# Performance work log

Hardware: AMD Instinct MI355X
Metric: run time of the kernel (lower is better)

## Reference

```python
import jax, jax.numpy as jnp
import numpy as np

N = 10000      # num nodes
E = 320000     # num edges
IN = 256       # in_dim
MP = 256       # mp_width
FL = 512       # fl_width
OUT = 64       # out_dim


def setup_inputs() -> dict:
    key = jax.random.key(0)
    ks = jax.random.split(key, 20)
    inp = {}
    inp["x"] = jax.random.normal(ks[0], (N, IN), dtype=jnp.float32)
    inp["edge_index"] = jax.random.randint(ks[1], (2, E), 0, N, dtype=jnp.int64)
    # iMP (frozen) linear layers: weight ~ N(0, 1) per nn.init.normal_(std=1.0)
    inp["mp_w0"] = jax.random.normal(ks[2], (IN, MP), dtype=jnp.float32)
    inp["mp_b0"] = jax.random.uniform(ks[3], (MP,), minval=-1.0, maxval=1.0) / np.sqrt(IN)
    inp["mp_w1"] = jax.random.normal(ks[4], (MP, MP), dtype=jnp.float32)
    inp["mp_b1"] = jax.random.uniform(ks[5], (MP,), minval=-1.0, maxval=1.0) / np.sqrt(MP)
    inp["mp_w2"] = jax.random.normal(ks[6], (MP, MP), dtype=jnp.float32)
    inp["mp_b2"] = jax.random.uniform(ks[7], (MP,), minval=-1.0, maxval=1.0) / np.sqrt(MP)
    # FC layers (torch default Linear init scale ~ 1/sqrt(fan_in))
    inp["fc_w0"] = jax.random.normal(ks[8], (MP, FL), dtype=jnp.float32) / np.sqrt(MP)
    inp["fc_b0"] = jnp.zeros((FL,), dtype=jnp.float32)
    inp["fc_w1"] = jax.random.normal(ks[9], (FL, FL), dtype=jnp.float32) / np.sqrt(FL)
    inp["fc_b1"] = jnp.zeros((FL,), dtype=jnp.float32)
    # injection projections
    inp["inj_w0"] = jax.random.normal(ks[10], (MP, FL), dtype=jnp.float32) / np.sqrt(MP)
    inp["inj_b0"] = jnp.zeros((FL,), dtype=jnp.float32)
    inp["inj_w1"] = jax.random.normal(ks[11], (MP, FL), dtype=jnp.float32) / np.sqrt(MP)
    inp["inj_b1"] = jnp.zeros((FL,), dtype=jnp.float32)
    inp["alpha"] = jnp.array(1.0, dtype=jnp.float32)
    inp["out_w"] = jax.random.normal(ks[12], (FL, OUT), dtype=jnp.float32) / np.sqrt(FL)
    inp["out_b"] = jnp.zeros((OUT,), dtype=jnp.float32)
    return inp


def _imp(x, w, b, row, col, deg_inv):
    # h = relu(W x); h /= deg; Ah = scatter_add over row of h[col]
    h = jax.nn.relu(x @ w + b) * deg_inv[:, None]      # [N, out]
    return jnp.zeros_like(h).at[row].add(h[col])       # gather + scatter-add


def reference(x, edge_index, mp_w0, mp_b0, mp_w1, mp_b1, mp_w2, mp_b2,
              fc_w0, fc_b0, fc_w1, fc_b1, inj_w0, inj_b0, inj_w1, inj_b1,
              alpha, out_w, out_b):
    row, col = edge_index[0], edge_index[1]
    deg = jax.ops.segment_sum(jnp.ones((E,), x.dtype), col, num_segments=N)
    # nodes with deg==0 never appear in col so clamping does not change output
    deg_inv = 1.0 / jnp.maximum(deg, 1.0)

    h = _imp(x, mp_w0, mp_b0, row, col, deg_inv)
    h = _imp(h, mp_w1, mp_b1, row, col, deg_inv)
    h = _imp(h, mp_w2, mp_b2, row, col, deg_inv)

    x_inject = h
    h = alpha * (jax.nn.relu(h) @ fc_w0 + fc_b0) + (x_inject @ inj_w0 + inj_b0)
    h = alpha * (jax.nn.relu(h) @ fc_w1 + fc_b1) + (x_inject @ inj_w1 + inj_b1)
    return h @ out_w + out_b
```

## Files before the change

kernel.cpp:

```cpp
#include <hip/hip_runtime.h>

#define N_NODES 10000
#define N_EDGES 320000
#define MPAD 10112
#define NBIN 10048
#define CAP 128
#define EBLKS 157
#define PREP_BLOCKS 512
#define PREP_TOT 1148480L

typedef unsigned short u16;
typedef short bf16x8 __attribute__((ext_vector_type(8)));
typedef float f32x4 __attribute__((ext_vector_type(4)));

__device__ __forceinline__ u16 f2b(float f) {
  unsigned u = __builtin_bit_cast(unsigned, f);
  unsigned r = u + 0x7fffu + ((u >> 16) & 1u);
  return (u16)(r >> 16);
}
__device__ __forceinline__ unsigned pack2(float a, float b) {
  return (unsigned)f2b(a) | ((unsigned)f2b(b) << 16);
}
__device__ __forceinline__ float blo(unsigned u) { return __builtin_bit_cast(float, u << 16); }
__device__ __forceinline__ float bhi(unsigned u) { return __builtin_bit_cast(float, u & 0xffff0000u); }

struct PP {
  const float *x; const int *ei;
  const float *w0, *w1, *w2, *fcw0, *injw0, *fcw1, *injw1, *outw;
  const float *fcb0, *injb0, *fcb1, *injb1, *alpha, *outb;
  u16 *xb, *w0t, *w1t, *w2t, *wc1t, *wft;
  float *bias1, *bf;
  int *cursor, *deg, *csr;
};

__global__ __launch_bounds__(256) void prep_place(PP P) {
  const int tid = threadIdx.x, bid = blockIdx.x;

  if (bid < EBLKS) {
    const int e0 = bid * 2048;
#pragma unroll
    for (int j = 0; j < 2048; j += 256) {
      int e = e0 + j + tid;
      if (e < N_EDGES) {
        int r = P.ei[e];
        int c = P.ei[N_EDGES + e];
        int pos = atomicAdd(&P.cursor[r], 1);
        if (pos < CAP) P.csr[r * CAP + pos] = c;
        atomicAdd(&P.deg[c], 1);
      }
    }
    return;
  }

  const float alpha = P.alpha[0];
  const long stride = (long)PREP_BLOCKS * 256;
  for (long ii = (long)(bid - EBLKS) * 256 + tid; ii < PREP_TOT; ii += stride) {
    long i = ii;
    if (i < 640000L) {
      float4 v = ((const float4*)P.x)[i];
      uint2 o;
      o.x = pack2(v.x, v.y);
      o.y = pack2(v.z, v.w);
      *(uint2*)(P.xb + 4 * i) = o;
      continue;
    }
    i -= 640000L;
    if (i < 65536) { P.w0t[i] = f2b(P.w0[(i & 255) * 256 + (i >> 8)]); continue; }
    i -= 65536;
    if (i < 65536) { P.w1t[i] = f2b(P.w1[(i & 255) * 256 + (i >> 8)]); continue; }
    i -= 65536;
    if (i < 65536) { P.w2t[i] = f2b(P.w2[(i & 255) * 256 + (i >> 8)]); continue; }
    i -= 65536;
    if (i < 262144) {
      int n = (int)(i >> 9), k = (int)(i & 511);
      float v = (k < 256) ? alpha * P.fcw0[k * 512 + n] : P.injw0[(k - 256) * 512 + n];
      P.wc1t[i] = f2b(v); continue;
    }
    i -= 262144;
    if (i < 49152) {
      int n = (int)(i & 63), k = (int)(i >> 6);
      const float* fr = (k < 512) ? P.fcw1 + (size_t)k * 512
                                  : P.injw1 + (size_t)(k - 512) * 512;
      float a0 = 0.f, a1 = 0.f, a2 = 0.f, a3 = 0.f;
#pragma unroll 4
      for (int j = 0; j < 512; j += 4) {
        float4 f = *(const float4*)(fr + j);
        a0 += f.x * P.outw[(j + 0) * 64 + n];
        a1 += f.y * P.outw[(j + 1) * 64 + n];
        a2 += f.z * P.outw[(j + 2) * 64 + n];
        a3 += f.w * P.outw[(j + 3) * 64 + n];
      }
      float acc = (a0 + a1) + (a2 + a3);
      if (k < 512) acc *= alpha;
      P.wft[n * 768 + k] = f2b(acc);
      continue;
    }
    i -= 49152;
    if (i < 64) {
      float acc = P.outb[i];
#pragma unroll 8
      for (int j = 0; j < 512; ++j)
        acc += (alpha * P.fcb1[j] + P.injb1[j]) * P.outw[j * 64 + i];
      P.bf[i] = acc;
      continue;
    }
    i -= 64;
    if (i < 512) { P.bias1[i] = alpha * P.fcb0[i] + P.injb0[i]; continue; }
  }
}

template<int K, bool RELU, bool SCALE, bool F32OUT>
__global__ __launch_bounds__(128) void gemm64(
    const u16* __restrict__ A, int lda,
    const u16* __restrict__ Bt,
    const float* __restrict__ bias,
    const int* __restrict__ deg,
    u16* __restrict__ Cb, float* __restrict__ Cf, int ldc)
{
  __shared__ u16 As[64 * 72];
  __shared__ u16 Bs[64 * 72];
  const int tid = threadIdx.x;
  const int m0 = blockIdx.x * 64;
  const int n0 = blockIdx.y * 64;
  const int wave = tid >> 6;
  const int lane = tid & 63;
  const int wr = wave * 32;
  const int lm = lane & 15;
  const int koff = (lane >> 4) * 8;

  const int srow = tid >> 2;
  const int scol = (tid & 3) * 16;
  const u16* Ag0 = A + (size_t)(m0 + srow) * lda + scol;
  const u16* Ag1 = A + (size_t)(m0 + srow + 32) * lda + scol;
  const u16* Bg0 = Bt + (size_t)(n0 + srow) * K + scol;
  const u16* Bg1 = Bt + (size_t)(n0 + srow + 32) * K + scol;
  u16* Asw0 = &As[srow * 72 + scol];
  u16* Asw1 = &As[(srow + 32) * 72 + scol];
  u16* Bsw0 = &Bs[srow * 72 + scol];
  u16* Bsw1 = &Bs[(srow + 32) * 72 + scol];

  f32x4 acc[2][4] = {};

  int4 pa0 = *(const int4*)(Ag0),     pa1 = *(const int4*)(Ag0 + 8);
  int4 pa2 = *(const int4*)(Ag1),     pa3 = *(const int4*)(Ag1 + 8);
  int4 pb0 = *(const int4*)(Bg0),     pb1 = *(const int4*)(Bg0 + 8);
  int4 pb2 = *(const int4*)(Bg1),     pb3 = *(const int4*)(Bg1 + 8);

#pragma unroll
  for (int kb = 0; kb < K; kb += 64) {
    __syncthreads();
    *(int4*)Asw0 = pa0; *(int4*)(Asw0 + 8) = pa1;
    *(int4*)Asw1 = pa2; *(int4*)(Asw1 + 8) = pa3;
    *(int4*)Bsw0 = pb0; *(int4*)(Bsw0 + 8) = pb1;
    *(int4*)Bsw1 = pb2; *(int4*)(Bsw1 + 8) = pb3;
    __syncthreads();
    if (kb + 64 < K) {
      pa0 = *(const int4*)(Ag0 + kb + 64); pa1 = *(const int4*)(Ag0 + kb + 72);
      pa2 = *(const int4*)(Ag1 + kb + 64); pa3 = *(const int4*)(Ag1 + kb + 72);
      pb0 = *(const int4*)(Bg0 + kb + 64); pb1 = *(const int4*)(Bg0 + kb + 72);
      pb2 = *(const int4*)(Bg1 + kb + 64); pb3 = *(const int4*)(Bg1 + kb + 72);
    }
#pragma unroll
    for (int ks = 0; ks < 2; ++ks) {
      bf16x8 af[2], bf[4];
#pragma unroll
      for (int mi = 0; mi < 2; ++mi)
        af[mi] = *(const bf16x8*)&As[(wr + mi * 16 + lm) * 72 + ks * 32 + koff];
#pragma unroll
      for (int ni = 0; ni < 4; ++ni)
        bf[ni] = *(const bf16x8*)&Bs[(ni * 16 + lm) * 72 + ks * 32 + koff];
#pragma unroll
      for (int mi = 0; mi < 2; ++mi)
#pragma unroll
        for (int ni = 0; ni < 4; ++ni)
          acc[mi][ni] = __builtin_amdgcn_mfma_f32_16x16x32_bf16(af[mi], bf[ni], acc[mi][ni], 0, 0, 0);
    }
  }

  const int q4 = (lane >> 4) * 4;
#pragma unroll
  for (int mi = 0; mi < 2; ++mi) {
#pragma unroll
    for (int ni = 0; ni < 4; ++ni) {
      const int gc = n0 + ni * 16 + lm;
      const float bv = bias[gc];
#pragma unroll
      for (int r = 0; r < 4; ++r) {
        const int gr = m0 + wr + mi * 16 + q4 + r;
        float v = acc[mi][ni][r] + bv;
        if (RELU) v = fmaxf(v, 0.f);
        if (SCALE) v *= 1.0f / fmaxf((float)deg[gr], 1.0f);
        if (F32OUT) {
          if (gr < N_NODES) Cf[(size_t)gr * ldc + gc] = v;
        } else {
          Cb[(size_t)gr * ldc + gc] = f2b(v);
        }
      }
    }
  }
}

__global__ __launch_bounds__(128) void gemm_fold(
    const u16* __restrict__ Ar,
    const u16* __restrict__ Ah,
    const u16* __restrict__ Bt,
    const float* __restrict__ bias,
    float* __restrict__ Cf)
{
  const int K = 768;
  __shared__ u16 As[64 * 72];
  __shared__ u16 Bs[64 * 72];
  const int tid = threadIdx.x;
  const int m0 = blockIdx.x * 64;
  const int n0 = 0;
  const int wave = tid >> 6;
  const int lane = tid & 63;
  const int wr = wave * 32;
  const int lm = lane & 15;
  const int koff = (lane >> 4) * 8;

  const int srow = tid >> 2;
  const int scol = (tid & 3) * 16;
  const int ar0 = m0 + srow, ar1 = m0 + srow + 32;
  auto aptr = [&](int row, int col) -> const u16* {
    return (col < 512) ? Ar + (size_t)row * 512 + col
                       : Ah + (size_t)row * 512 + (col - 512);
  };
  const u16* Bg0 = Bt + (size_t)(n0 + srow) * K + scol;
  const u16* Bg1 = Bt + (size_t)(n0 + srow + 32) * K + scol;
  u16* Asw0 = &As[srow * 72 + scol];
  u16* Asw1 = &As[(srow + 32) * 72 + scol];
  u16* Bsw0 = &Bs[srow * 72 + scol];
  u16* Bsw1 = &Bs[(srow + 32) * 72 + scol];

  f32x4 acc[2][4] = {};

  int4 pa0 = *(const int4*)aptr(ar0, scol);
  int4 pa1 = *(const int4*)aptr(ar0, scol + 8);
  int4 pa2 = *(const int4*)aptr(ar1, scol);
  int4 pa3 = *(const int4*)aptr(ar1, scol + 8);
  int4 pb0 = *(const int4*)(Bg0), pb1 = *(const int4*)(Bg0 + 8);
  int4 pb2 = *(const int4*)(Bg1), pb3 = *(const int4*)(Bg1 + 8);

#pragma unroll
  for (int kb = 0; kb < K; kb += 64) {
    __syncthreads();
    *(int4*)Asw0 = pa0; *(int4*)(Asw0 + 8) = pa1;
    *(int4*)Asw1 = pa2; *(int4*)(Asw1 + 8) = pa3;
    *(int4*)Bsw0 = pb0; *(int4*)(Bsw0 + 8) = pb1;
    *(int4*)Bsw1 = pb2; *(int4*)(Bsw1 + 8) = pb3;
    __syncthreads();
    if (kb + 64 < K) {
      int c = kb + 64 + scol;
      pa0 = *(const int4*)aptr(ar0, c);
      pa1 = *(const int4*)aptr(ar0, c + 8);
      pa2 = *(const int4*)aptr(ar1, c);
      pa3 = *(const int4*)aptr(ar1, c + 8);
      pb0 = *(const int4*)(Bg0 + kb + 64); pb1 = *(const int4*)(Bg0 + kb + 72);
      pb2 = *(const int4*)(Bg1 + kb + 64); pb3 = *(const int4*)(Bg1 + kb + 72);
    }
#pragma unroll
    for (int ks = 0; ks < 2; ++ks) {
      bf16x8 af[2], bf[4];
#pragma unroll
      for (int mi = 0; mi < 2; ++mi)
        af[mi] = *(const bf16x8*)&As[(wr + mi * 16 + lm) * 72 + ks * 32 + koff];
#pragma unroll
      for (int ni = 0; ni < 4; ++ni)
        bf[ni] = *(const bf16x8*)&Bs[(ni * 16 + lm) * 72 + ks * 32 + koff];
#pragma unroll
      for (int mi = 0; mi < 2; ++mi)
#pragma unroll
        for (int ni = 0; ni < 4; ++ni)
          acc[mi][ni] = __builtin_amdgcn_mfma_f32_16x16x32_bf16(af[mi], bf[ni], acc[mi][ni], 0, 0, 0);
    }
  }

  const int q4 = (lane >> 4) * 4;
#pragma unroll
  for (int mi = 0; mi < 2; ++mi) {
#pragma unroll
    for (int ni = 0; ni < 4; ++ni) {
      const int gc = ni * 16 + lm;
      const float bv = bias[gc];
#pragma unroll
      for (int r = 0; r < 4; ++r) {
        const int gr = m0 + wr + mi * 16 + q4 + r;
        if (gr < N_NODES) Cf[(size_t)gr * 64 + gc] = acc[mi][ni][r] + bv;
      }
    }
  }
}

__global__ __launch_bounds__(256) void aggregate(
    const u16* __restrict__ tmp, const int* __restrict__ cnt,
    const int* __restrict__ csr, u16* __restrict__ out0,
    u16* __restrict__ A1, int mode)
{
  const int wv = threadIdx.x >> 6;
  const int lane = threadIdx.x & 63;
  const int r = blockIdx.x * 4 + wv;
  const int half = lane >> 5;
  const int q = lane & 31;
  int n = cnt[r]; if (n > CAP) n = CAP;
  const int beg = r * CAP, end = beg + n;
  const size_t feat = (size_t)q * 16;
  const char* tb = (const char*)tmp;

  float s0 = 0.f, s1 = 0.f, s2 = 0.f, s3 = 0.f, s4 = 0.f, s5 = 0.f, s6 = 0.f, s7 = 0.f;
  int i = beg;
  for (; i + 8 <= end; i += 8) {
    uint4 v[4];
#pragma unroll
    for (int j = 0; j < 4; ++j)
      v[j] = *(const uint4*)(tb + (size_t)csr[i + 2 * j + half] * 512 + feat);
#pragma unroll
    for (int j = 0; j < 4; ++j) {
      s0 += blo(v[j].x); s1 += bhi(v[j].x); s2 += blo(v[j].y); s3 += bhi(v[j].y);
      s4 += blo(v[j].z); s5 += bhi(v[j].z); s6 += blo(v[j].w); s7 += bhi(v[j].w);
    }
  }
  for (; i < end; i += 2) {
    int id = i + half;
    if (id < end) {
      uint4 v = *(const uint4*)(tb + (size_t)csr[id] * 512 + feat);
      s0 += blo(v.x); s1 += bhi(v.x); s2 += blo(v.y); s3 += bhi(v.y);
      s4 += blo(v.z); s5 += bhi(v.z); s6 += blo(v.w); s7 += bhi(v.w);
    }
  }
  const int src = lane ^ 32;
  s0 += __shfl(s0, src, 64); s1 += __shfl(s1, src, 64);
  s2 += __shfl(s2, src, 64); s3 += __shfl(s3, src, 64);
  s4 += __shfl(s4, src, 64); s5 += __shfl(s5, src, 64);
  s6 += __shfl(s6, src, 64); s7 += __shfl(s7, src, 64);

  if (half == 0) {
    uint4 pv;
    pv.x = pack2(s0, s1); pv.y = pack2(s2, s3);
    pv.z = pack2(s4, s5); pv.w = pack2(s6, s7);
    if (mode == 0) {
      *(uint4*)((char*)out0 + (size_t)r * 512 + feat) = pv;
    } else {
      uint4 pr;
      pr.x = pack2(fmaxf(s0, 0.f), fmaxf(s1, 0.f));
      pr.y = pack2(fmaxf(s2, 0.f), fmaxf(s3, 0.f));
      pr.z = pack2(fmaxf(s4, 0.f), fmaxf(s5, 0.f));
      pr.w = pack2(fmaxf(s6, 0.f), fmaxf(s7, 0.f));
      *(uint4*)((char*)A1 + (size_t)r * 1024 + feat) = pr;
      *(uint4*)((char*)A1 + (size_t)r * 1024 + 512 + feat) = pv;
    }
  }
}

extern "C" void kernel_launch(void* const* d_in, const int* in_sizes, int n_in,
                              void* d_out, int out_size, void* d_ws, size_t ws_size,
                              hipStream_t stream) {
  const int* ei = (const int*)d_in[1];

  char* p = (char*)d_ws;
  auto carve = [&](size_t bytes) -> void* {
    void* r = (void*)p;
    p += (bytes + 255) & ~(size_t)255;
    return r;
  };
  int*   deg     = (int*)carve(MPAD * 4);
  int*   cursor  = (int*)carve(NBIN * 4);
  int*   csr     = (int*)carve((size_t)NBIN * CAP * 4);
  float* bias1   = (float*)carve(512 * 4);
  float* bf      = (float*)carve(64 * 4);
  u16* xb    = (u16*)carve((size_t)MPAD * 256 * 2);
  u16* w0t   = (u16*)carve(65536 * 2);
  u16* w1t   = (u16*)carve(65536 * 2);
  u16* w2t   = (u16*)carve(65536 * 2);
  u16* wc1t  = (u16*)carve(262144 * 2);
  u16* wft   = (u16*)carve(49152 * 2);
  u16* tmp   = (u16*)carve((size_t)MPAD * 256 * 2);
  u16* h     = (u16*)carve((size_t)MPAD * 256 * 2);
  u16* cat1  = (u16*)carve((size_t)MPAD * 512 * 2);
  u16* relu1 = (u16*)carve((size_t)MPAD * 512 * 2);

  PP pp;
  pp.x = (const float*)d_in[0];
  pp.ei = ei;
  pp.w0 = (const float*)d_in[2];
  pp.w1 = (const float*)d_in[4];
  pp.w2 = (const float*)d_in[6];
  pp.fcw0 = (const float*)d_in[8];
  pp.fcw1 = (const float*)d_in[10];
  pp.injw0 = (const float*)d_in[12];
  pp.injw1 = (const float*)d_in[14];
  pp.outw = (const float*)d_in[17];
  pp.fcb0 = (const float*)d_in[9];
  pp.injb0 = (const float*)d_in[13];
  pp.fcb1 = (const float*)d_in[11];
  pp.injb1 = (const float*)d_in[15];
  pp.alpha = (const float*)d_in[16];
  pp.outb = (const float*)d_in[18];
  pp.xb = xb; pp.w0t = w0t; pp.w1t = w1t; pp.w2t = w2t;
  pp.wc1t = wc1t; pp.wft = wft;
  pp.bias1 = bias1; pp.bf = bf;
  pp.cursor = cursor; pp.deg = deg; pp.csr = csr;

  const float* mp_b0 = (const float*)d_in[3];
  const float* mp_b1 = (const float*)d_in[5];
  const float* mp_b2 = (const float*)d_in[7];
  float* out = (float*)d_out;

  hipMemsetAsync(deg, 0, (size_t)(MPAD + NBIN) * 4, stream);
  prep_place<<<EBLKS + PREP_BLOCKS, 256, 0, stream>>>(pp);

  dim3 gmp(MPAD / 64, 4), gfc(MPAD / 64, 8), go(MPAD / 64, 1);
  gemm64<256, true, true, false><<<gmp, 128, 0, stream>>>(xb, 256, w0t, mp_b0, deg, tmp, nullptr, 256);
  aggregate<<<2500, 256, 0, stream>>>(tmp, cursor, csr, h, nullptr, 0);
  gemm64<256, true, true, false><<<gmp, 128, 0, stream>>>(h, 256, w1t, mp_b1, deg, tmp, nullptr, 256);
  aggregate<<<2500, 256, 0, stream>>>(tmp, cursor, csr, h, nullptr, 0);
  gemm64<256, true, true, false><<<gmp, 128, 0, stream>>>(h, 256, w2t, mp_b2, deg, tmp, nullptr, 256);
  aggregate<<<2500, 256, 0, stream>>>(tmp, cursor, csr, nullptr, cat1, 1);
  gemm64<512, true, false, false><<<gfc, 128, 0, stream>>>(cat1, 512, wc1t, bias1, nullptr, relu1, nullptr, 512);
  gemm_fold<<<go, 128, 0, stream>>>(relu1, cat1 + 256, wft, bf, out);
}
```

Before: 236.0 us.

## Fuse fp32-to-bf16 input conversion into first GEMM and shrink CSR to u16

```diff
diff --git a/kernel.cpp b/kernel.cpp
--- a/kernel.cpp
+++ b/kernel.cpp
@@ -7,7 +7,7 @@
 #define CAP 128
 #define EBLKS 157
 #define PREP_BLOCKS 512
-#define PREP_TOT 1148480L
+#define PREP_TOT 508480L
 
 typedef unsigned short u16;
 typedef short bf16x8 __attribute__((ext_vector_type(8)));
@@ -23,14 +23,20 @@
 }
 __device__ __forceinline__ float blo(unsigned u) { return __builtin_bit_cast(float, u << 16); }
 __device__ __forceinline__ float bhi(unsigned u) { return __builtin_bit_cast(float, u & 0xffff0000u); }
+__device__ __forceinline__ int4 cvt16(float4 a, float4 b) {
+  int4 r;
+  r.x = (int)pack2(a.x, a.y); r.y = (int)pack2(a.z, a.w);
+  r.z = (int)pack2(b.x, b.y); r.w = (int)pack2(b.z, b.w);
+  return r;
+}
 
 struct PP {
   const float *x; const int *ei;
   const float *w0, *w1, *w2, *fcw0, *injw0, *fcw1, *injw1, *outw;
   const float *fcb0, *injb0, *fcb1, *injb1, *alpha, *outb;
-  u16 *xb, *w0t, *w1t, *w2t, *wc1t, *wft;
+  u16 *w0t, *w1t, *w2t, *wc1t, *wft;
   float *bias1, *bf;
-  int *cursor, *deg, *csr;
+  int *cursor, *deg; u16 *csr;
 };
 
 __global__ __launch_bounds__(256) void prep_place(PP P) {
@@ -44,9 +50,9 @@
       if (e < N_EDGES) {
         int r = P.ei[e];
         int c = P.ei[N_EDGES + e];
+        atomicAdd(&P.deg[c], 1);
         int pos = atomicAdd(&P.cursor[r], 1);
-        if (pos < CAP) P.csr[r * CAP + pos] = c;
-        atomicAdd(&P.deg[c], 1);
+        if (pos < CAP) P.csr[r * CAP + pos] = (u16)c;
       }
     }
     return;
@@ -56,15 +62,6 @@
   const long stride = (long)PREP_BLOCKS * 256;
   for (long ii = (long)(bid - EBLKS) * 256 + tid; ii < PREP_TOT; ii += stride) {
     long i = ii;
-    if (i < 640000L) {
-      float4 v = ((const float4*)P.x)[i];
-      uint2 o;
-      o.x = pack2(v.x, v.y);
-      o.y = pack2(v.z, v.w);
-      *(uint2*)(P.xb + 4 * i) = o;
-      continue;
-    }
-    i -= 640000L;
     if (i < 65536) { P.w0t[i] = f2b(P.w0[(i & 255) * 256 + (i >> 8)]); continue; }
     i -= 65536;
     if (i < 65536) { P.w1t[i] = f2b(P.w1[(i & 255) * 256 + (i >> 8)]); continue; }
@@ -109,9 +106,9 @@
   }
 }
 
-template<int K, bool RELU, bool SCALE, bool F32OUT>
+template<int K, bool RELU, bool SCALE, bool F32OUT, bool AF32>
 __global__ __launch_bounds__(128) void gemm64(
-    const u16* __restrict__ A, int lda,
+    const void* __restrict__ Av, int lda,
     const u16* __restrict__ Bt,
     const float* __restrict__ bias,
     const int* __restrict__ deg,
@@ -130,8 +127,17 @@
 
   const int srow = tid >> 2;
   const int scol = (tid & 3) * 16;
-  const u16* Ag0 = A + (size_t)(m0 + srow) * lda + scol;
-  const u16* Ag1 = A + (size_t)(m0 + srow + 32) * lda + scol;
+  const u16 *Ag0 = nullptr, *Ag1 = nullptr;
+  const float *Af0 = nullptr, *Af1 = nullptr;
+  if constexpr (AF32) {
+    const int ar0 = min(m0 + srow, N_NODES - 1);
+    const int ar1 = min(m0 + srow + 32, N_NODES - 1);
+    Af0 = (const float*)Av + (size_t)ar0 * lda + scol;
+    Af1 = (const float*)Av + (size_t)ar1 * lda + scol;
+  } else {
+    Ag0 = (const u16*)Av + (size_t)(m0 + srow) * lda + scol;
+    Ag1 = (const u16*)Av + (size_t)(m0 + srow + 32) * lda + scol;
+  }
   const u16* Bg0 = Bt + (size_t)(n0 + srow) * K + scol;
   const u16* Bg1 = Bt + (size_t)(n0 + srow + 32) * K + scol;
   u16* Asw0 = &As[srow * 72 + scol];
@@ -141,8 +147,18 @@
 
   f32x4 acc[2][4] = {};
 
-  int4 pa0 = *(const int4*)(Ag0),     pa1 = *(const int4*)(Ag0 + 8);
-  int4 pa2 = *(const int4*)(Ag1),     pa3 = *(const int4*)(Ag1 + 8);
+  int4 pa0, pa1, pa2, pa3;
+  if constexpr (AF32) {
+    float4 f0 = *(const float4*)(Af0),     f1 = *(const float4*)(Af0 + 4);
+    float4 f2 = *(const float4*)(Af0 + 8), f3 = *(const float4*)(Af0 + 12);
+    float4 g0 = *(const float4*)(Af1),     g1 = *(const float4*)(Af1 + 4);
+    float4 g2 = *(const float4*)(Af1 + 8), g3 = *(const float4*)(Af1 + 12);
+    pa0 = cvt16(f0, f1); pa1 = cvt16(f2, f3);
+    pa2 = cvt16(g0, g1); pa3 = cvt16(g2, g3);
+  } else {
+    pa0 = *(const int4*)(Ag0); pa1 = *(const int4*)(Ag0 + 8);
+    pa2 = *(const int4*)(Ag1); pa3 = *(const int4*)(Ag1 + 8);
+  }
   int4 pb0 = *(const int4*)(Bg0),     pb1 = *(const int4*)(Bg0 + 8);
   int4 pb2 = *(const int4*)(Bg1),     pb3 = *(const int4*)(Bg1 + 8);
 
@@ -155,8 +171,19 @@
     *(int4*)Bsw1 = pb2; *(int4*)(Bsw1 + 8) = pb3;
     __syncthreads();
     if (kb + 64 < K) {
-      pa0 = *(const int4*)(Ag0 + kb + 64); pa1 = *(const int4*)(Ag0 + kb + 72);
-      pa2 = *(const int4*)(Ag1 + kb + 64); pa3 = *(const int4*)(Ag1 + kb + 72);
+      if constexpr (AF32) {
+        const float* a0 = Af0 + kb + 64;
+        const float* a1 = Af1 + kb + 64;
+        float4 f0 = *(const float4*)(a0),     f1 = *(const float4*)(a0 + 4);
+        float4 f2 = *(const float4*)(a0 + 8), f3 = *(const float4*)(a0 + 12);
+        float4 g0 = *(const float4*)(a1),     g1 = *(const float4*)(a1 + 4);
+        float4 g2 = *(const float4*)(a1 + 8), g3 = *(const float4*)(a1 + 12);
+        pa0 = cvt16(f0, f1); pa1 = cvt16(f2, f3);
+        pa2 = cvt16(g0, g1); pa3 = cvt16(g2, g3);
+      } else {
+        pa0 = *(const int4*)(Ag0 + kb + 64); pa1 = *(const int4*)(Ag0 + kb + 72);
+        pa2 = *(const int4*)(Ag1 + kb + 64); pa3 = *(const int4*)(Ag1 + kb + 72);
+      }
       pb0 = *(const int4*)(Bg0 + kb + 64); pb1 = *(const int4*)(Bg0 + kb + 72);
       pb2 = *(const int4*)(Bg1 + kb + 64); pb3 = *(const int4*)(Bg1 + kb + 72);
     }
@@ -294,7 +321,7 @@
 
 __global__ __launch_bounds__(256) void aggregate(
     const u16* __restrict__ tmp, const int* __restrict__ cnt,
-    const int* __restrict__ csr, u16* __restrict__ out0,
+    const u16* __restrict__ csr, u16* __restrict__ out0,
     u16* __restrict__ A1, int mode)
 {
   const int wv = threadIdx.x >> 6;
@@ -365,10 +392,9 @@
   };
   int*   deg     = (int*)carve(MPAD * 4);
   int*   cursor  = (int*)carve(NBIN * 4);
-  int*   csr     = (int*)carve((size_t)NBIN * CAP * 4);
+  u16*   csr     = (u16*)carve((size_t)NBIN * CAP * 2);
   float* bias1   = (float*)carve(512 * 4);
   float* bf      = (float*)carve(64 * 4);
-  u16* xb    = (u16*)carve((size_t)MPAD * 256 * 2);
   u16* w0t   = (u16*)carve(65536 * 2);
   u16* w1t   = (u16*)carve(65536 * 2);
   u16* w2t   = (u16*)carve(65536 * 2);
@@ -396,7 +422,7 @@
   pp.injb1 = (const float*)d_in[15];
   pp.alpha = (const float*)d_in[16];
   pp.outb = (const float*)d_in[18];
-  pp.xb = xb; pp.w0t = w0t; pp.w1t = w1t; pp.w2t = w2t;
+  pp.w0t = w0t; pp.w1t = w1t; pp.w2t = w2t;
   pp.wc1t = wc1t; pp.wft = wft;
   pp.bias1 = bias1; pp.bf = bf;
   pp.cursor = cursor; pp.deg = deg; pp.csr = csr;
@@ -410,12 +436,12 @@
   prep_place<<<EBLKS + PREP_BLOCKS, 256, 0, stream>>>(pp);
 
   dim3 gmp(MPAD / 64, 4), gfc(MPAD / 64, 8), go(MPAD / 64, 1);
-  gemm64<256, true, true, false><<<gmp, 128, 0, stream>>>(xb, 256, w0t, mp_b0, deg, tmp, nullptr, 256);
+  gemm64<256, true, true, false, true ><<<gmp, 128, 0, stream>>>(pp.x, 256, w0t, mp_b0, deg, tmp, nullptr, 256);
   aggregate<<<2500, 256, 0, stream>>>(tmp, cursor, csr, h, nullptr, 0);
-  gemm64<256, true, true, false><<<gmp, 128, 0, stream>>>(h, 256, w1t, mp_b1, deg, tmp, nullptr, 256);
+  gemm64<256, true, true, false, false><<<gmp, 128, 0, stream>>>(h, 256, w1t, mp_b1, deg, tmp, nullptr, 256);
   aggregate<<<2500, 256, 0, stream>>>(tmp, cursor, csr, h, nullptr, 0);
-  gemm64<256, true, true, false><<<gmp, 128, 0, stream>>>(h, 256, w2t, mp_b2, deg, tmp, nullptr, 256);
+  gemm64<256, true, true, false, false><<<gmp, 128, 0, stream>>>(h, 256, w2t, mp_b2, deg, tmp, nullptr, 256);
   aggregate<<<2500, 256, 0, stream>>>(tmp, cursor, csr, nullptr, cat1, 1);
-  gemm64<512, true, false, false><<<gfc, 128, 0, stream>>>(cat1, 512, wc1t, bias1, nullptr, relu1, nullptr, 512);
+  gemm64<512, true, false, false, false><<<gfc, 128, 0, stream>>>(cat1, 512, wc1t, bias1, nullptr, relu1, nullptr, 512);
   gemm_fold<<<go, 128, 0, stream>>>(relu1, cat1 + 256, wft, bf, out);
 }
```

Measured after the change: 237.6 us. No clear change (+0.7%).
